# Kernel tuning notes

Hardware: AMD Instinct MI355X
Metric: run time of the kernel (lower is better)

The kernel has to match this reference:

```python
import jax, jax.numpy as jnp
import numpy as np

N, E = 50000, 800000
CIN, COUT = 128, 128
FORDER = 4          # cascade of GegConv with K = 1..FORDER
ALPHA = 0.5         # Gegenbauer alpha
LAMBDA_MAX = 2.0    # default lambda_max => L_hat = -(D^-1/2 A D^-1/2)


def setup_inputs() -> dict:
    key = jax.random.key(0)
    ks = jax.random.split(key, 8)
    x = jax.random.normal(ks[0], (N, CIN), dtype=jnp.float32)
    edge_index = jax.random.randint(ks[1], (2, E), 0, N, dtype=jnp.int32)
    edge_weight = jax.random.uniform(ks[2], (E,), dtype=jnp.float32)
    wstd = np.sqrt(2.0 / (CIN + COUT)).astype(np.float32)  # glorot-ish
    inp = {"x": x, "edge_index": edge_index, "edge_weight": edge_weight}
    for i in range(FORDER):
        K = i + 1
        inp[f"W{K}"] = wstd * jax.random.normal(ks[3 + i], (K, CIN, COUT), dtype=jnp.float32)
        inp[f"b{K}"] = jnp.zeros((COUT,), dtype=jnp.float32)
    return inp


def _sym_norm(edge_index, edge_weight):
    # ChebConv-style symmetric normalization of adjacency weights
    row, col = edge_index[0], edge_index[1]
    deg = jnp.zeros((N,), edge_weight.dtype).at[row].add(edge_weight)
    dis = jnp.where(deg > 0, jax.lax.rsqrt(jnp.where(deg > 0, deg, 1.0)), 0.0)
    return dis[row] * edge_weight * dis[col]


def reference(x, edge_index, edge_weight, W1, W2, W3, W4, b1, b2, b3, b4):
    row, col = edge_index[0], edge_index[1]
    norm = _sym_norm(edge_index, edge_weight)

    def prop(h):  # A_hat h = D^-1/2 A D^-1/2 h  (scatter-add over edges)
        return jnp.zeros_like(h).at[col].add(norm[:, None] * h[row])

    def lhat(h):  # (2/lambda_max) * (I - A_hat) h - h
        return (2.0 / LAMBDA_MAX) * (h - prop(h)) - h

    # Shared Gegenbauer basis Tx_0..Tx_{FORDER-1}:
    # C_0 = 1, C_1 = 2*alpha*z, C_k = (2(k+a-1) z C_{k-1} - (k+2a-2) C_{k-2}) / k
    Tx = [x]
    if FORDER > 1:
        Tx.append(2.0 * ALPHA * lhat(x))
    for k in range(2, FORDER):
        Tk = (2.0 * (k + ALPHA - 1.0) / k) * lhat(Tx[-1]) \
             - ((k + 2.0 * ALPHA - 2.0) / k) * Tx[-2]
        Tx.append(Tk)

    Ws = [W1, W2, W3, W4]
    bs = [b1, b2, b3, b4]
    outs = []
    for i in range(FORDER):
        K = i + 1
        basis = jnp.stack(Tx[:K])                       # [K, N, CIN]
        h = jnp.einsum('knc,kcd->nd', basis, Ws[i]) + bs[i]
        outs.append(jax.nn.relu(h))                     # dropout = identity (eval mode)
    return tuple(outs)
```

## Files before the change

kernel.cpp:

```cpp
#include <hip/hip_runtime.h>
#include <cstddef>
#include <cstdint>

#define NN 50000
#define NE 800000
#define CH 128

#define NBUCK 782
#define BH 200
#define EPB 4000
#define MH (NBUCK * BH)
#define G1 ((MH + 255) / 256)

#define DR 8
#define DRS 6250
#define DC 50
#define DCE 16000
#define DBLK 448

#define FIXS 8388608.0f

typedef unsigned int u32;
typedef unsigned short u16;
typedef unsigned long long u64;
typedef __attribute__((ext_vector_type(4))) unsigned int u32x4;
typedef __attribute__((ext_vector_type(8))) unsigned short u16x8;
typedef __attribute__((ext_vector_type(8))) __bf16 bf16x8;
typedef __attribute__((ext_vector_type(4))) float f32x4;

__device__ __forceinline__ u32 bf_rne(float f) {
  u32 u = __float_as_uint(f);
  return (u + 0x7FFFu + ((u >> 16) & 1u)) >> 16;
}
__device__ __forceinline__ u32 pack_bf2(float lo, float hi) {
  return bf_rne(lo) | (bf_rne(hi) << 16);
}
__device__ __forceinline__ float bflo(u32 v) { return __uint_as_float(v << 16); }
__device__ __forceinline__ float bfhi(u32 v) { return __uint_as_float(v & 0xFFFF0000u); }

__device__ __forceinline__ int wave_scan_incl(int v) {
  int lane = threadIdx.x & 63;
#pragma unroll
  for (int d = 1; d < 64; d <<= 1) {
    int u = __shfl_up(v, d, 64);
    if (lane >= d) v += u;
  }
  return v;
}

__device__ __forceinline__ int block_scan_incl(int v, int* wsum) {
  int t = threadIdx.x, lane = t & 63, wid = t >> 6;
  int incl = wave_scan_incl(v);
  if (lane == 63) wsum[wid] = incl;
  __syncthreads();
  int add = 0;
#pragma unroll
  for (int w = 0; w < 3; ++w) add += (w < wid) ? wsum[w] : 0;
  return incl + add;
}

__global__ __launch_bounds__(256) void kB_deg(const int* __restrict__ ei, const float* __restrict__ ew,
                                              int* __restrict__ part, int* __restrict__ hist) {
  __shared__ u32 lh[DRS];
  __shared__ int ch[NBUCK];
  const int bid = blockIdx.x;
  const int low3 = bid & 7;
  const int q = bid >> 3;
  const int r = q & 7;
  const int chi = q >> 3;
  const int c = chi * 8 + low3;
  if (c >= DC) return;
  const int t = threadIdx.x;
  for (int i = t; i < DRS; i += 256) lh[i] = 0u;
  if (r < 4) for (int i = t; i < NBUCK; i += 256) ch[i] = 0;
  __syncthreads();
  const int base = r * DRS;
  const int4* rows4 = (const int4*)(ei + c * DCE);
  const float4* ws4 = (const float4*)(ew + c * DCE);
  for (int v = t; v < DCE / 4; v += 256) {
    int4 rv = rows4[v];
    float4 wv = ws4[v];
    unsigned rel;
    rel = (unsigned)(rv.x - base); if (rel < (unsigned)DRS) atomicAdd(&lh[rel], (u32)(wv.x * FIXS + 0.5f));
    rel = (unsigned)(rv.y - base); if (rel < (unsigned)DRS) atomicAdd(&lh[rel], (u32)(wv.y * FIXS + 0.5f));
    rel = (unsigned)(rv.z - base); if (rel < (unsigned)DRS) atomicAdd(&lh[rel], (u32)(wv.z * FIXS + 0.5f));
    rel = (unsigned)(rv.w - base); if (rel < (unsigned)DRS) atomicAdd(&lh[rel], (u32)(wv.w * FIXS + 0.5f));
  }
  if (r < 4) {
    const int cb = 4 * c + r;
    const int4* cols4 = (const int4*)(ei + NE + cb * EPB);
    for (int v = t; v < EPB / 4; v += 256) {
      int4 cv = cols4[v];
      atomicAdd(&ch[cv.x >> 6], 1);
      atomicAdd(&ch[cv.y >> 6], 1);
      atomicAdd(&ch[cv.z >> 6], 1);
      atomicAdd(&ch[cv.w >> 6], 1);
    }
  }
  __syncthreads();
  int* dst = part + (size_t)c * NN + base;
  for (int i = t; i < DRS; i += 256) dst[i] = (int)lh[i];
  if (r < 4) {
    const int cb = 4 * c + r;
    for (int i = t; i < NBUCK; i += 256) hist[i * BH + cb] = ch[i];
  }
}

__global__ __launch_bounds__(256) void k_degred(const int* __restrict__ part, float* __restrict__ dis) {
  int i = blockIdx.x * 256 + threadIdx.x;
  if (i >= NN) return;
  int s = 0;
#pragma unroll 10
  for (int c = 0; c < DC; ++c) s += part[(size_t)c * NN + i];
  dis[i] = (s > 0) ? rsqrtf((float)s * (1.0f / FIXS)) : 0.f;
}

__global__ __launch_bounds__(256) void k_scan1(const int* __restrict__ hist, int* __restrict__ partials) {
  __shared__ int wsum[4];
  int i = blockIdx.x * 256 + threadIdx.x;
  int v = (i < MH) ? hist[i] : 0;
  int incl = block_scan_incl(v, wsum);
  if (threadIdx.x == 255) partials[blockIdx.x] = incl;
}

__global__ __launch_bounds__(256) void k_scan2(int* __restrict__ partials) {
  __shared__ int wsum[4];
  __shared__ int carrys;
  const int t = threadIdx.x;
  int carry = 0;
#pragma unroll
  for (int r = 0; r < 3; ++r) {
    int idx = r * 256 + t;
    int v = (idx < G1) ? partials[idx] : 0;
    int incl = block_scan_incl(v, wsum);
    if (idx < G1) partials[idx] = carry + incl - v;
    if (t == 255) carrys = incl;
    __syncthreads();
    carry += carrys;
    __syncthreads();
  }
}

__global__ __launch_bounds__(256) void k_scan3(int* __restrict__ hist, const int* __restrict__ partials) {
  __shared__ int wsum[4];
  int i = blockIdx.x * 256 + threadIdx.x;
  int v = (i < MH) ? hist[i] : 0;
  int incl = block_scan_incl(v, wsum);
  if (i < MH) hist[i] = incl - v + partials[blockIdx.x];
}

__global__ __launch_bounds__(256) void kC(const int* __restrict__ ei, const float* __restrict__ ew,
                                          const int* __restrict__ excl, u64* __restrict__ sorted) {
  __shared__ int lbase[NBUCK];
  __shared__ int lcnt[NBUCK];
  const int b = blockIdx.x, t = threadIdx.x;
  for (int i = t; i < NBUCK; i += 256) { lbase[i] = excl[i * BH + b]; lcnt[i] = 0; }
  __syncthreads();
  const int e0 = b * EPB;
  const int4* srcs4 = (const int4*)(ei + e0);
  const int4* cols4 = (const int4*)(ei + NE + e0);
  const float4* ws4 = (const float4*)(ew + e0);
  for (int v = t; v < EPB / 4; v += 256) {
    int4 sv = srcs4[v];
    int4 cv = cols4[v];
    float4 wv = ws4[v];
    int bk, rk;
    bk = cv.x >> 6; rk = atomicAdd(&lcnt[bk], 1);
    sorted[lbase[bk] + rk] = ((u64)__float_as_uint(wv.x) << 32) | ((u32)cv.x << 16) | (u32)sv.x;
    bk = cv.y >> 6; rk = atomicAdd(&lcnt[bk], 1);
    sorted[lbase[bk] + rk] = ((u64)__float_as_uint(wv.y) << 32) | ((u32)cv.y << 16) | (u32)sv.y;
    bk = cv.z >> 6; rk = atomicAdd(&lcnt[bk], 1);
    sorted[lbase[bk] + rk] = ((u64)__float_as_uint(wv.z) << 32) | ((u32)cv.z << 16) | (u32)sv.z;
    bk = cv.w >> 6; rk = atomicAdd(&lcnt[bk], 1);
    sorted[lbase[bk] + rk] = ((u64)__float_as_uint(wv.w) << 32) | ((u32)cv.w << 16) | (u32)sv.w;
  }
}

__global__ __launch_bounds__(256) void kD(const u64* __restrict__ sorted, const int* __restrict__ excl,
                                          const float* __restrict__ dis, int* __restrict__ rp,
                                          u64* __restrict__ meta) {
  __shared__ int h[64];
  __shared__ int cur[64];
  __shared__ float disc[64];
  const int b = blockIdx.x, t = threadIdx.x;
  const int seg0 = excl[b * BH];
  const int seg1 = (b + 1 < NBUCK) ? excl[(b + 1) * BH] : NE;
  if (t < 64) {
    h[t] = 0;
    int c = (b << 6) + t;
    disc[t] = (c < NN) ? dis[c] : 0.f;
  }
  __syncthreads();
  for (int p = seg0 + t; p < seg1; p += 256) {
    u32 lo = (u32)sorted[p];
    atomicAdd(&h[(lo >> 16) & 63], 1);
  }
  __syncthreads();
  if (t < 64) {
    int v = h[t];
    int incl = wave_scan_incl(v);
    int excl_l = incl - v;
    cur[t] = seg0 + excl_l;
    int c = (b << 6) + t;
    if (c < NN) rp[c] = seg0 + excl_l;
    else if (c == NN) rp[NN] = seg0 + excl_l;
  }
  __syncthreads();
  for (int p = seg0 + t; p < seg1; p += 256) {
    u64 v = sorted[p];
    u32 lo = (u32)v;
    int src = lo & 0xFFFF;
    int local = (lo >> 16) & 63;
    float ewf = __uint_as_float((u32)(v >> 32));
    int q = atomicAdd(&cur[local], 1);
    float w = ewf * dis[src] * disc[local];
    meta[q] = ((u64)__float_as_uint(w) << 32) | (u32)src;
  }
}

#define XB_BLOCKS 12500
__global__ __launch_bounds__(256) void k_conv(const float* __restrict__ x, u32* __restrict__ xb,
                                              const float* __restrict__ W0, const float* __restrict__ W1,
                                              const float* __restrict__ W2, const float* __restrict__ W3,
                                              u16* __restrict__ Wp) {
  if (blockIdx.x < XB_BLOCKS) {
    int i = blockIdx.x * 256 + threadIdx.x;
    if (i < NN * 64) {
      float2 f = ((const float2*)x)[i];
      xb[i] = pack_bf2(f.x, f.y);
    }
    return;
  }
  int t = (blockIdx.x - XB_BLOCKS) * 256 + threadIdx.x;
  if (t >= 10 * 4 * 8 * 64) return;
  int lane = t & 63, cb = (t >> 6) & 7, kb = (t >> 9) & 3, m = t >> 11;
  const float* Wb; int io;
  if (m == 0)      { Wb = W0; io = 0; }
  else if (m < 3)  { Wb = W1; io = m - 1; }
  else if (m < 6)  { Wb = W2; io = m - 3; }
  else             { Wb = W3; io = m - 6; }
  const float* s = Wb + (size_t)io * CH * CH;
  int c  = cb * 16 + (lane & 15);
  int k0 = kb * 32 + (lane >> 4) * 8;
  u16* o = Wp + (size_t)t * 8;
#pragma unroll
  for (int e = 0; e < 8; ++e) o[e] = (u16)bf_rne(s[(k0 + e) * CH + c]);
}

__global__ __launch_bounds__(256) void k_prop_bf(const int* __restrict__ rp, const u64* __restrict__ meta,
                                                 const u32* __restrict__ h, const u32* __restrict__ other,
                                                 u32* __restrict__ outb,
                                                 const float coefP, const float coefO) {
  const int node = blockIdx.x * 4 + (threadIdx.x >> 6);
  const int lane = threadIdx.x & 63;
  const int g = lane >> 4;
  const int cq = lane & 15;
  if (node >= NN) return;
  const int j0 = rp[node], j1 = rp[node + 1];
  float a0 = 0.f, a1 = 0.f, a2 = 0.f, a3 = 0.f, a4 = 0.f, a5 = 0.f, a6 = 0.f, a7 = 0.f;
  if (j0 < j1) {
    int ji = j0 + g;
    u64 mnext = meta[(ji < j1) ? ji : (j1 - 1)];
#pragma unroll 4
    for (int j = j0; j < j1; j += 4) {
      const u64 m = mnext;
      const int jn = j + 4 + g;
      mnext = meta[(jn < j1) ? jn : (j1 - 1)];
      const bool act = (j + g) < j1;
      const float w = act ? __uint_as_float((u32)(m >> 32)) : 0.f;
      const u32 src = (u32)m & 0xFFFFu;
      u32x4 v = *(const u32x4*)&h[(size_t)src * 64 + cq * 4];
      a0 = fmaf(w, bflo(v.x), a0); a1 = fmaf(w, bfhi(v.x), a1);
      a2 = fmaf(w, bflo(v.y), a2); a3 = fmaf(w, bfhi(v.y), a3);
      a4 = fmaf(w, bflo(v.z), a4); a5 = fmaf(w, bfhi(v.z), a5);
      a6 = fmaf(w, bflo(v.w), a6); a7 = fmaf(w, bfhi(v.w), a7);
    }
  }
  a0 += __shfl_xor(a0, 16); a1 += __shfl_xor(a1, 16);
  a2 += __shfl_xor(a2, 16); a3 += __shfl_xor(a3, 16);
  a4 += __shfl_xor(a4, 16); a5 += __shfl_xor(a5, 16);
  a6 += __shfl_xor(a6, 16); a7 += __shfl_xor(a7, 16);
  a0 += __shfl_xor(a0, 32); a1 += __shfl_xor(a1, 32);
  a2 += __shfl_xor(a2, 32); a3 += __shfl_xor(a3, 32);
  a4 += __shfl_xor(a4, 32); a5 += __shfl_xor(a5, 32);
  a6 += __shfl_xor(a6, 32); a7 += __shfl_xor(a7, 32);
  if (lane < 16) {
    const size_t oi = (size_t)node * 64 + cq * 4;
    float o0 = 0.f, o1 = 0.f, o2 = 0.f, o3 = 0.f, o4 = 0.f, o5 = 0.f, o6 = 0.f, o7 = 0.f;
    if (other != nullptr) {
      u32x4 ov = *(const u32x4*)&other[oi];
      o0 = bflo(ov.x); o1 = bfhi(ov.x); o2 = bflo(ov.y); o3 = bfhi(ov.y);
      o4 = bflo(ov.z); o5 = bfhi(ov.z); o6 = bflo(ov.w); o7 = bfhi(ov.w);
    }
    u32x4 r;
    r.x = pack_bf2(fmaf(coefP, a0, coefO * o0), fmaf(coefP, a1, coefO * o1));
    r.y = pack_bf2(fmaf(coefP, a2, coefO * o2), fmaf(coefP, a3, coefO * o3));
    r.z = pack_bf2(fmaf(coefP, a4, coefO * o4), fmaf(coefP, a5, coefO * o5));
    r.w = pack_bf2(fmaf(coefP, a6, coefO * o6), fmaf(coefP, a7, coefO * o7));
    *(u32x4*)&outb[oi] = r;
  }
}

__global__ __launch_bounds__(256, 4) void k_gemm_all(
    const u16* __restrict__ xb, const u16* __restrict__ t1,
    const u16* __restrict__ t2, const u16* __restrict__ t3,
    const u16* __restrict__ Wp,
    const float* __restrict__ b0, const float* __restrict__ b1,
    const float* __restrict__ b2, const float* __restrict__ b3,
    float* __restrict__ out) {
  __shared__ __align__(16) char ldsb[2][8192];
  const int tid = threadIdx.x;
  const int w = tid >> 6, lane = tid & 63;
  const int rowg0 = blockIdx.x * 32;
  const u16* bases[4] = {xb, t1, t2, t3};
  const int mbase[4] = {0, 1, 3, 6};

  const int c0 = tid,        r_0 = c0 >> 4, s_0 = (c0 & 15) << 4;
  const int c1 = 256 + tid,  r_1 = c1 >> 4, s_1 = (c1 & 15) << 4;

  f32x4 acc[4][2][2];
#pragma unroll
  for (int k = 0; k < 4; ++k)
#pragma unroll
    for (int rf = 0; rf < 2; ++rf)
#pragma unroll
      for (int c = 0; c < 2; ++c) acc[k][rf][c] = (f32x4){0.f, 0.f, 0.f, 0.f};

  {
    u16x8 v0 = {0,0,0,0,0,0,0,0}, v1 = {0,0,0,0,0,0,0,0};
    if (rowg0 + r_0 < NN) v0 = *(const u16x8*)((const char*)bases[0] + (size_t)(rowg0 + r_0) * 256 + s_0);
    if (rowg0 + r_1 < NN) v1 = *(const u16x8*)((const char*)bases[0] + (size_t)(rowg0 + r_1) * 256 + s_1);
    *(u16x8*)(&ldsb[0][r_0 * 256 + (s_0 ^ ((r_0 & 7) << 4))]) = v0;
    *(u16x8*)(&ldsb[0][r_1 * 256 + (s_1 ^ ((r_1 & 7) << 4))]) = v1;
  }
  __syncthreads();

#pragma unroll
  for (int i = 0; i < 4; ++i) {
    u16x8 nv0 = {0,0,0,0,0,0,0,0}, nv1 = {0,0,0,0,0,0,0,0};
    if (i < 3) {
      if (rowg0 + r_0 < NN) nv0 = *(const u16x8*)((const char*)bases[i + 1] + (size_t)(rowg0 + r_0) * 256 + s_0);
      if (rowg0 + r_1 < NN) nv1 = *(const u16x8*)((const char*)bases[i + 1] + (size_t)(rowg0 + r_1) * 256 + s_1);
    }

    const char* tile = ldsb[i & 1];
#pragma unroll
    for (int ks = 0; ks < 4; ++ks) {
      const int kb = ks * 64 + ((lane >> 4) << 4);
      const int r0 = (lane & 15), r1 = 16 + (lane & 15);
      const bf16x8 a0 = __builtin_bit_cast(bf16x8,
          *(const u16x8*)(tile + r0 * 256 + (kb ^ ((r0 & 7) << 4))));
      const bf16x8 a1 = __builtin_bit_cast(bf16x8,
          *(const u16x8*)(tile + r1 * 256 + (kb ^ ((r1 & 7) << 4))));
#pragma unroll
      for (int k = 3; k >= 0; --k) {
        if (k < i) continue;
        const int m = mbase[k] + i;
        const bf16x8 bf0 = __builtin_bit_cast(bf16x8,
            *(const u16x8*)(Wp + (size_t)((m * 4 + ks) * 8 + (w * 2 + 0)) * 512 + lane * 8));
        const bf16x8 bf1 = __builtin_bit_cast(bf16x8,
            *(const u16x8*)(Wp + (size_t)((m * 4 + ks) * 8 + (w * 2 + 1)) * 512 + lane * 8));
        acc[k][0][0] = __builtin_amdgcn_mfma_f32_16x16x32_bf16(a0, bf0, acc[k][0][0], 0, 0, 0);
        acc[k][1][0] = __builtin_amdgcn_mfma_f32_16x16x32_bf16(a1, bf0, acc[k][1][0], 0, 0, 0);
        acc[k][0][1] = __builtin_amdgcn_mfma_f32_16x16x32_bf16(a0, bf1, acc[k][0][1], 0, 0, 0);
        acc[k][1][1] = __builtin_amdgcn_mfma_f32_16x16x32_bf16(a1, bf1, acc[k][1][1], 0, 0, 0);
      }
    }
    if (i < 3) {
      char* nb = ldsb[(i + 1) & 1];
      *(u16x8*)(&nb[r_0 * 256 + (s_0 ^ ((r_0 & 7) << 4))]) = nv0;
      *(u16x8*)(&nb[r_1 * 256 + (s_1 ^ ((r_1 & 7) << 4))]) = nv1;
    }
    __syncthreads();
  }

  const float* biases[4] = {b0, b1, b2, b3};
  const int colb = w * 32;
#pragma unroll
  for (int k = 0; k < 4; ++k) {
    const float bv0 = biases[k][colb + (lane & 15)];
    const float bv1 = biases[k][colb + 16 + (lane & 15)];
    float* ok = out + (size_t)k * NN * CH;
#pragma unroll
    for (int rf = 0; rf < 2; ++rf) {
#pragma unroll
      for (int j = 0; j < 4; ++j) {
        const int row = rowg0 + rf * 16 + ((lane >> 4) << 2) + j;
        if (row < NN) {
          ok[(size_t)row * CH + colb + (lane & 15)]      = fmaxf(acc[k][rf][0][j] + bv0, 0.f);
          ok[(size_t)row * CH + colb + 16 + (lane & 15)] = fmaxf(acc[k][rf][1][j] + bv1, 0.f);
        }
      }
    }
  }
}

static inline size_t align256(size_t x) { return (x + 255) & ~(size_t)255; }

extern "C" void kernel_launch(void* const* d_in, const int* in_sizes, int n_in,
                              void* d_out, int out_size, void* d_ws, size_t ws_size,
                              hipStream_t stream) {
  const float* x  = (const float*)d_in[0];
  const int*   ei = (const int*)d_in[1];
  const float* ew = (const float*)d_in[2];
  const float* W[4]  = {(const float*)d_in[3], (const float*)d_in[5],
                        (const float*)d_in[7], (const float*)d_in[9]};
  const float* bs[4] = {(const float*)d_in[4], (const float*)d_in[6],
                        (const float*)d_in[8], (const float*)d_in[10]};
  float* out = (float*)d_out;

  char* ws = (char*)d_ws;
  size_t off = 0;
  auto alloc = [&](size_t bytes) -> void* { void* p = ws + off; off = align256(off + bytes); return p; };
  float* dis      = (float*)alloc(sizeof(float) * NN);
  int*   rp       = (int*)alloc(sizeof(int) * (NN + 1));
  int*   hist     = (int*)alloc(sizeof(int) * MH);
  int*   partials = (int*)alloc(sizeof(int) * 1024);
  int*   part     = (int*)alloc(sizeof(int) * (size_t)DC * NN);
  u64*   sorted   = (u64*)alloc(sizeof(u64) * NE);
  u64*   meta     = (u64*)alloc(sizeof(u64) * NE);
  u32*   xb       = (u32*)alloc(sizeof(u32) * (size_t)NN * 64);
  u32*   t1b      = (u32*)alloc(sizeof(u32) * (size_t)NN * 64);
  u32*   t2b      = (u32*)alloc(sizeof(u32) * (size_t)NN * 64);
  u32*   t3b      = (u32*)alloc(sizeof(u32) * (size_t)NN * 64);
  u16*   Wp       = (u16*)alloc(sizeof(u16) * 10 * 4 * 8 * 64 * 8);
  (void)ws_size; (void)in_sizes; (void)n_in; (void)out_size;

  kB_deg<<<DBLK, 256, 0, stream>>>(ei, ew, part, hist);
  k_degred<<<(NN + 255) / 256, 256, 0, stream>>>(part, dis);

  k_scan1<<<G1, 256, 0, stream>>>(hist, partials);
  k_scan2<<<1, 256, 0, stream>>>(partials);
  k_scan3<<<G1, 256, 0, stream>>>(hist, partials);
  kC<<<BH, 256, 0, stream>>>(ei, ew, hist, sorted);
  kD<<<NBUCK, 256, 0, stream>>>(sorted, hist, dis, rp, meta);

  k_conv<<<XB_BLOCKS + 80, 256, 0, stream>>>(x, xb, W[0], W[1], W[2], W[3], Wp);

  k_prop_bf<<<12500, 256, 0, stream>>>(rp, meta, xb, nullptr, t1b, -1.f, 0.f);
  k_prop_bf<<<12500, 256, 0, stream>>>(rp, meta, t1b, xb, t2b, -1.5f, -0.5f);
  k_prop_bf<<<12500, 256, 0, stream>>>(rp, meta, t2b, t1b, t3b, -5.f / 3.f, -2.f / 3.f);

  k_gemm_all<<<(NN + 31) / 32, 256, 0, stream>>>(
      (const u16*)xb, (const u16*)t1b, (const u16*)t2b, (const u16*)t3b,
      Wp, bs[0], bs[1], bs[2], bs[3], out);
}
```

Measured before the change: 189.2 us.

## Merge degree, column histogram and bf16 conversion into one front kernel

Folds the degree partial sums, the column-bucket histogram and the x/W bf16 conversion into a single launch, and merges the degree reduction into the final scan kernel. This cuts kernel launches and lets independent work overlap. It also splits the histogram into its own 800 blocks of 1000 edges, so kC now runs with 800 blocks instead of 200. The trade-off is a 4x larger histogram, which makes the three scan passes process more data.

```diff
diff --git a/kernel.cpp b/kernel.cpp
--- a/kernel.cpp
+++ b/kernel.cpp
@@ -7,10 +7,11 @@
 #define CH 128
 
 #define NBUCK 782
-#define BH 200
-#define EPB 4000
+#define BH 800
+#define EPB 1000
 #define MH (NBUCK * BH)
 #define G1 ((MH + 255) / 256)
+#define S2R ((G1 + 255) / 256)
 
 #define DR 8
 #define DRS 6250
@@ -19,6 +20,9 @@
 #define DBLK 448
 
 #define FIXS 8388608.0f
+
+#define XB_BLOCKS 12500
+#define FRONT_BLOCKS (DBLK + BH + XB_BLOCKS + 80)
 
 typedef unsigned int u32;
 typedef unsigned short u16;
@@ -59,36 +63,49 @@
   return incl + add;
 }
 
-__global__ __launch_bounds__(256) void kB_deg(const int* __restrict__ ei, const float* __restrict__ ew,
-                                              int* __restrict__ part, int* __restrict__ hist) {
-  __shared__ u32 lh[DRS];
-  __shared__ int ch[NBUCK];
+__global__ __launch_bounds__(256) void k_front(const int* __restrict__ ei, const float* __restrict__ ew,
+                                               int* __restrict__ part, int* __restrict__ hist,
+                                               const float* __restrict__ x, u32* __restrict__ xb,
+                                               const float* __restrict__ W0, const float* __restrict__ W1,
+                                               const float* __restrict__ W2, const float* __restrict__ W3,
+                                               u16* __restrict__ Wp) {
+  __shared__ u32 smem[DRS];
   const int bid = blockIdx.x;
-  const int low3 = bid & 7;
-  const int q = bid >> 3;
-  const int r = q & 7;
-  const int chi = q >> 3;
-  const int c = chi * 8 + low3;
-  if (c >= DC) return;
   const int t = threadIdx.x;
-  for (int i = t; i < DRS; i += 256) lh[i] = 0u;
-  if (r < 4) for (int i = t; i < NBUCK; i += 256) ch[i] = 0;
-  __syncthreads();
-  const int base = r * DRS;
-  const int4* rows4 = (const int4*)(ei + c * DCE);
-  const float4* ws4 = (const float4*)(ew + c * DCE);
-  for (int v = t; v < DCE / 4; v += 256) {
-    int4 rv = rows4[v];
-    float4 wv = ws4[v];
-    unsigned rel;
-    rel = (unsigned)(rv.x - base); if (rel < (unsigned)DRS) atomicAdd(&lh[rel], (u32)(wv.x * FIXS + 0.5f));
-    rel = (unsigned)(rv.y - base); if (rel < (unsigned)DRS) atomicAdd(&lh[rel], (u32)(wv.y * FIXS + 0.5f));
-    rel = (unsigned)(rv.z - base); if (rel < (unsigned)DRS) atomicAdd(&lh[rel], (u32)(wv.z * FIXS + 0.5f));
-    rel = (unsigned)(rv.w - base); if (rel < (unsigned)DRS) atomicAdd(&lh[rel], (u32)(wv.w * FIXS + 0.5f));
-  }
-  if (r < 4) {
-    const int cb = 4 * c + r;
-    const int4* cols4 = (const int4*)(ei + NE + cb * EPB);
+
+  if (bid < DBLK) {
+    const int low3 = bid & 7;
+    const int q = bid >> 3;
+    const int r = q & 7;
+    const int chi = q >> 3;
+    const int c = chi * 8 + low3;
+    if (c >= DC) return;
+    for (int i = t; i < DRS; i += 256) smem[i] = 0u;
+    __syncthreads();
+    const int base = r * DRS;
+    const int4* rows4 = (const int4*)(ei + c * DCE);
+    const float4* ws4 = (const float4*)(ew + c * DCE);
+    for (int v = t; v < DCE / 4; v += 256) {
+      int4 rv = rows4[v];
+      float4 wv = ws4[v];
+      unsigned rel;
+      rel = (unsigned)(rv.x - base); if (rel < (unsigned)DRS) atomicAdd(&smem[rel], (u32)(wv.x * FIXS + 0.5f));
+      rel = (unsigned)(rv.y - base); if (rel < (unsigned)DRS) atomicAdd(&smem[rel], (u32)(wv.y * FIXS + 0.5f));
+      rel = (unsigned)(rv.z - base); if (rel < (unsigned)DRS) atomicAdd(&smem[rel], (u32)(wv.z * FIXS + 0.5f));
+      rel = (unsigned)(rv.w - base); if (rel < (unsigned)DRS) atomicAdd(&smem[rel], (u32)(wv.w * FIXS + 0.5f));
+    }
+    __syncthreads();
+    int* dst = part + (size_t)c * NN + base;
+    for (int i = t; i < DRS; i += 256) dst[i] = (int)smem[i];
+    return;
+  }
+
+  if (bid < DBLK + BH) {
+    const int b = bid - DBLK;
+    int* ch = (int*)smem;
+    for (int i = t; i < NBUCK; i += 256) ch[i] = 0;
+    __syncthreads();
+    const int4* cols4 = (const int4*)(ei + NE + b * EPB);
     for (int v = t; v < EPB / 4; v += 256) {
       int4 cv = cols4[v];
       atomicAdd(&ch[cv.x >> 6], 1);
@@ -96,23 +113,34 @@
       atomicAdd(&ch[cv.z >> 6], 1);
       atomicAdd(&ch[cv.w >> 6], 1);
     }
-  }
-  __syncthreads();
-  int* dst = part + (size_t)c * NN + base;
-  for (int i = t; i < DRS; i += 256) dst[i] = (int)lh[i];
-  if (r < 4) {
-    const int cb = 4 * c + r;
-    for (int i = t; i < NBUCK; i += 256) hist[i * BH + cb] = ch[i];
-  }
-}
-
-__global__ __launch_bounds__(256) void k_degred(const int* __restrict__ part, float* __restrict__ dis) {
-  int i = blockIdx.x * 256 + threadIdx.x;
-  if (i >= NN) return;
-  int s = 0;
-#pragma unroll 10
-  for (int c = 0; c < DC; ++c) s += part[(size_t)c * NN + i];
-  dis[i] = (s > 0) ? rsqrtf((float)s * (1.0f / FIXS)) : 0.f;
+    __syncthreads();
+    for (int i = t; i < NBUCK; i += 256) hist[i * BH + b] = ch[i];
+    return;
+  }
+
+  const int c2 = bid - (DBLK + BH);
+  if (c2 < XB_BLOCKS) {
+    int i = c2 * 256 + t;
+    if (i < NN * 64) {
+      float2 f = ((const float2*)x)[i];
+      xb[i] = pack_bf2(f.x, f.y);
+    }
+    return;
+  }
+  int tt = (c2 - XB_BLOCKS) * 256 + t;
+  if (tt >= 10 * 4 * 8 * 64) return;
+  int lane = tt & 63, cb = (tt >> 6) & 7, kb = (tt >> 9) & 3, m = tt >> 11;
+  const float* Wb; int io;
+  if (m == 0)      { Wb = W0; io = 0; }
+  else if (m < 3)  { Wb = W1; io = m - 1; }
+  else if (m < 6)  { Wb = W2; io = m - 3; }
+  else             { Wb = W3; io = m - 6; }
+  const float* s = Wb + (size_t)io * CH * CH;
+  int c  = cb * 16 + (lane & 15);
+  int k0 = kb * 32 + (lane >> 4) * 8;
+  u16* o = Wp + (size_t)tt * 8;
+#pragma unroll
+  for (int e = 0; e < 8; ++e) o[e] = (u16)bf_rne(s[(k0 + e) * CH + c]);
 }
 
 __global__ __launch_bounds__(256) void k_scan1(const int* __restrict__ hist, int* __restrict__ partials) {
@@ -129,7 +157,7 @@
   const int t = threadIdx.x;
   int carry = 0;
 #pragma unroll
-  for (int r = 0; r < 3; ++r) {
+  for (int r = 0; r < S2R; ++r) {
     int idx = r * 256 + t;
     int v = (idx < G1) ? partials[idx] : 0;
     int incl = block_scan_incl(v, wsum);
@@ -141,12 +169,23 @@
   }
 }
 
-__global__ __launch_bounds__(256) void k_scan3(int* __restrict__ hist, const int* __restrict__ partials) {
+__global__ __launch_bounds__(256) void k_mid(int* __restrict__ hist, const int* __restrict__ partials,
+                                             const int* __restrict__ part, float* __restrict__ dis) {
   __shared__ int wsum[4];
-  int i = blockIdx.x * 256 + threadIdx.x;
-  int v = (i < MH) ? hist[i] : 0;
-  int incl = block_scan_incl(v, wsum);
-  if (i < MH) hist[i] = incl - v + partials[blockIdx.x];
+  const int bid = blockIdx.x;
+  if (bid < G1) {
+    int i = bid * 256 + threadIdx.x;
+    int v = (i < MH) ? hist[i] : 0;
+    int incl = block_scan_incl(v, wsum);
+    if (i < MH) hist[i] = incl - v + partials[bid];
+    return;
+  }
+  int i = (bid - G1) * 256 + threadIdx.x;
+  if (i >= NN) return;
+  int s = 0;
+#pragma unroll 10
+  for (int c = 0; c < DC; ++c) s += part[(size_t)c * NN + i];
+  dis[i] = (s > 0) ? rsqrtf((float)s * (1.0f / FIXS)) : 0.f;
 }
 
 __global__ __launch_bounds__(256) void kC(const int* __restrict__ ei, const float* __restrict__ ew,
@@ -216,35 +255,6 @@
     float w = ewf * dis[src] * disc[local];
     meta[q] = ((u64)__float_as_uint(w) << 32) | (u32)src;
   }
-}
-
-#define XB_BLOCKS 12500
-__global__ __launch_bounds__(256) void k_conv(const float* __restrict__ x, u32* __restrict__ xb,
-                                              const float* __restrict__ W0, const float* __restrict__ W1,
-                                              const float* __restrict__ W2, const float* __restrict__ W3,
-                                              u16* __restrict__ Wp) {
-  if (blockIdx.x < XB_BLOCKS) {
-    int i = blockIdx.x * 256 + threadIdx.x;
-    if (i < NN * 64) {
-      float2 f = ((const float2*)x)[i];
-      xb[i] = pack_bf2(f.x, f.y);
-    }
-    return;
-  }
-  int t = (blockIdx.x - XB_BLOCKS) * 256 + threadIdx.x;
-  if (t >= 10 * 4 * 8 * 64) return;
-  int lane = t & 63, cb = (t >> 6) & 7, kb = (t >> 9) & 3, m = t >> 11;
-  const float* Wb; int io;
-  if (m == 0)      { Wb = W0; io = 0; }
-  else if (m < 3)  { Wb = W1; io = m - 1; }
-  else if (m < 6)  { Wb = W2; io = m - 3; }
-  else             { Wb = W3; io = m - 6; }
-  const float* s = Wb + (size_t)io * CH * CH;
-  int c  = cb * 16 + (lane & 15);
-  int k0 = kb * 32 + (lane >> 4) * 8;
-  u16* o = Wp + (size_t)t * 8;
-#pragma unroll
-  for (int e = 0; e < 8; ++e) o[e] = (u16)bf_rne(s[(k0 + e) * CH + c]);
 }
 
 __global__ __launch_bounds__(256) void k_prop_bf(const int* __restrict__ rp, const u64* __restrict__ meta,
@@ -415,7 +425,7 @@
   float* dis      = (float*)alloc(sizeof(float) * NN);
   int*   rp       = (int*)alloc(sizeof(int) * (NN + 1));
   int*   hist     = (int*)alloc(sizeof(int) * MH);
-  int*   partials = (int*)alloc(sizeof(int) * 1024);
+  int*   partials = (int*)alloc(sizeof(int) * 4096);
   int*   part     = (int*)alloc(sizeof(int) * (size_t)DC * NN);
   u64*   sorted   = (u64*)alloc(sizeof(u64) * NE);
   u64*   meta     = (u64*)alloc(sizeof(u64) * NE);
@@ -426,16 +436,14 @@
   u16*   Wp       = (u16*)alloc(sizeof(u16) * 10 * 4 * 8 * 64 * 8);
   (void)ws_size; (void)in_sizes; (void)n_in; (void)out_size;
 
-  kB_deg<<<DBLK, 256, 0, stream>>>(ei, ew, part, hist);
-  k_degred<<<(NN + 255) / 256, 256, 0, stream>>>(part, dis);
+  k_front<<<FRONT_BLOCKS, 256, 0, stream>>>(ei, ew, part, hist, x, xb,
+                                            W[0], W[1], W[2], W[3], Wp);
 
   k_scan1<<<G1, 256, 0, stream>>>(hist, partials);
   k_scan2<<<1, 256, 0, stream>>>(partials);
-  k_scan3<<<G1, 256, 0, stream>>>(hist, partials);
+  k_mid<<<G1 + (NN + 255) / 256, 256, 0, stream>>>(hist, partials, part, dis);
   kC<<<BH, 256, 0, stream>>>(ei, ew, hist, sorted);
   kD<<<NBUCK, 256, 0, stream>>>(sorted, hist, dis, rp, meta);
-
-  k_conv<<<XB_BLOCKS + 80, 256, 0, stream>>>(x, xb, W[0], W[1], W[2], W[3], Wp);
 
   k_prop_bf<<<12500, 256, 0, stream>>>(rp, meta, xb, nullptr, t1b, -1.f, 0.f);
   k_prop_bf<<<12500, 256, 0, stream>>>(rp, meta, t1b, xb, t2b, -1.5f, -0.5f);
```

New measurement: 192.7 us. Within noise of the previous version (+1.8%).
